# Performance work log

Hardware: AMD Instinct MI355X
Metric: run time of the kernel (lower is better)

Reference implementation:

```python
import jax, jax.numpy as jnp
import numpy as np

D_MODEL = 768
HEADS = 12
D_HEAD = D_MODEL // HEADS
D_DYNA = 768
EPS = 1e-5
B, SP, SI = 16, 256, 1024


def _layernorm(x, g, b):
    mu = jnp.mean(x, axis=-1, keepdims=True)
    var = jnp.var(x, axis=-1, keepdims=True)
    return (x - mu) * jax.lax.rsqrt(var + EPS) * g + b


def _mha(q, k, v, wq, bq, wk, bk, wv, bv, wo, bo):
    # weights stored [d_in, d_out]; torch Linear math y = x @ W^T + b is
    # equivalent with transposed storage.
    B_ = q.shape[0]
    qh = (q @ wq + bq).reshape(B_, -1, HEADS, D_HEAD)
    kh = (k @ wk + bk).reshape(B_, -1, HEADS, D_HEAD)
    vh = (v @ wv + bv).reshape(B_, -1, HEADS, D_HEAD)
    scores = jnp.einsum('bqhd,bkhd->bhqk', qh, kh) / np.sqrt(D_HEAD).astype(np.float32)
    attn = jax.nn.softmax(scores, axis=-1)  # dropout disabled (eval)
    out = jnp.einsum('bhqk,bkhd->bqhd', attn, vh).reshape(B_, -1, D_MODEL)
    return out @ wo + bo


def setup_inputs() -> dict:
    key = jax.random.key(0)
    ks = iter(jax.random.split(key, 40))
    s = 0.02
    d = {
        'image': jax.random.normal(next(ks), (B, SI, D_MODEL), jnp.float32),
        'prompt': jax.random.normal(next(ks), (B, SP, D_MODEL), jnp.float32),
        'posi': jax.random.normal(next(ks), (B, SI, D_MODEL), jnp.float32),
        'posp': jax.random.normal(next(ks), (B, SP, D_MODEL), jnp.float32),
    }
    for ln in ('ln_p1', 'ln_p2', 'ln_p3', 'ln_i1'):
        d[ln + '_g'] = jnp.ones((D_MODEL,), jnp.float32)
        d[ln + '_b'] = jnp.zeros((D_MODEL,), jnp.float32)
    for pre in ('pp', 'pi'):
        for nm in ('q', 'k', 'v', 'o'):
            d[f'{pre}_w{nm}'] = s * jax.random.normal(next(ks), (D_MODEL, D_MODEL), jnp.float32)
            d[f'{pre}_b{nm}'] = jnp.zeros((D_MODEL,), jnp.float32)
    d['ff_w1'] = s * jax.random.normal(next(ks), (D_MODEL, D_MODEL), jnp.float32)
    d['ff_b1'] = jnp.zeros((D_MODEL,), jnp.float32)
    d['ff_w2'] = s * jax.random.normal(next(ks), (D_MODEL, D_DYNA), jnp.float32)
    d['ff_b2'] = jnp.zeros((D_DYNA,), jnp.float32)
    return d


def reference(image, prompt, posi, posp,
              ln_p1_g, ln_p1_b, ln_p2_g, ln_p2_b, ln_p3_g, ln_p3_b, ln_i1_g, ln_i1_b,
              pp_wq, pp_bq, pp_wk, pp_bk, pp_wv, pp_bv, pp_wo, pp_bo,
              pi_wq, pi_bq, pi_wk, pi_bk, pi_wv, pi_bv, pi_wo, pi_bo,
              ff_w1, ff_b1, ff_w2, ff_b2):
    prompt0 = prompt + posp
    xp = _layernorm(prompt0, ln_p1_g, ln_p1_b)
    xp = _mha(xp, xp, xp, pp_wq, pp_bq, pp_wk, pp_bk, pp_wv, pp_bv, pp_wo, pp_bo)
    prompt = prompt + xp  # dropout_p1 is identity in eval
    xp = _layernorm(prompt + prompt0, ln_p2_g, ln_p2_b)
    xi = _layernorm(image + posi, ln_i1_g, ln_i1_b)
    xp = _mha(xp, xi, xi, pi_wq, pi_bq, pi_wk, pi_bk, pi_wv, pi_bv, pi_wo, pi_bo)
    prompt = prompt + xp  # dropout_p2 identity
    xp = _layernorm(prompt + prompt0, ln_p3_g, ln_p3_b)
    xp = jax.nn.relu(xp @ ff_w1 + ff_b1) @ ff_w2 + ff_b2
    return xp
```

## Files before the change

### kernel.cpp

```cpp
#include <hip/hip_runtime.h>
#include <hip/hip_bf16.h>
#include <stdint.h>
#include <math.h>

#define D_MODEL 768
#define HEADS 12
#define D_HEAD 64
#define BATCH 16
#define SP 256
#define SI 1024
#define NP (BATCH * SP)
#define NI (BATCH * SI)

#define GLOBAL_AS __attribute__((address_space(1)))
#define LDS_AS    __attribute__((address_space(3)))

typedef __attribute__((ext_vector_type(8))) short  frag_ab;
typedef __attribute__((ext_vector_type(4))) float  frag_cd;

static __device__ __forceinline__ ushort f2bf(float f) {
  __hip_bfloat16 h = __float2bfloat16(f);
  return *(ushort*)&h;
}
static __device__ __forceinline__ float bf2f(ushort u) {
  return __bfloat162float(*(__hip_bfloat16*)&u);
}
static __device__ __forceinline__ bool probe_bf(const uint32_t* p) {
  return p[0] == 0x3F803F80u;
}

struct Prep {
  const void* wsrc[10]; ushort* wdst[10];
  const void* vsrc[18]; float* vdst;
};

__global__ __launch_bounds__(256) void prep_kernel(Prep p, const uint32_t* probe) {
  const bool isbf = probe_bf(probe);
  const int z = blockIdx.z;
  if (z < 10) {
    __shared__ float tile[32][33];
    const int tx = threadIdx.x & 31, ty = threadIdx.x >> 5;
    const int x0 = blockIdx.x * 32, y0 = blockIdx.y * 32;
    const void* src = p.wsrc[z];
    ushort* dst = p.wdst[z];
#pragma unroll
    for (int i = 0; i < 4; i++) {
      const int y = y0 + ty + i * 8;
      float v;
      if (isbf) v = bf2f(((const ushort*)src)[(size_t)y * 768 + x0 + tx]);
      else      v = ((const float*)src)[(size_t)y * 768 + x0 + tx];
      tile[ty + i * 8][tx] = v;
    }
    __syncthreads();
#pragma unroll
    for (int i = 0; i < 4; i++) {
      const int row = x0 + ty + i * 8;
      const int col = y0 + tx;
      dst[(size_t)row * 768 + col] = f2bf(tile[tx][ty + i * 8]);
    }
  } else {
    const int idx = (blockIdx.y * 24 + blockIdx.x) * 256 + threadIdx.x;
    if (idx < 18 * 768) {
      const int e = idx / 768, i = idx - e * 768;
      float v;
      if (isbf) v = bf2f(((const ushort*)p.vsrc[e])[i]);
      else      v = ((const float*)p.vsrc[e])[i];
      p.vdst[idx] = v;
    }
  }
}

struct LNJob {
  const void* a; const void* b;
  const float* g; const float* be;
  float* sum_out; ushort* ln_out;
  int nrows; int abf;
};

__global__ __launch_bounds__(256) void add_ln_wave(LNJob J0, LNJob J1, const uint32_t* probe) {
  const int w = threadIdx.x >> 6, lane = threadIdx.x & 63;
  int row = blockIdx.x * 4 + w;
  LNJob j = (row < J0.nrows) ? J0 : J1;
  if (row >= J0.nrows) row -= J0.nrows;
  if (row >= j.nrows) return;
  const size_t base = (size_t)row * D_MODEL;
  const bool isbf = j.abf && probe_bf(probe);
  float x[12];
#pragma unroll
  for (int k = 0; k < 3; k++) {
    const int c = k * 256 + lane * 4;
    if (isbf) {
      const uint2 ua = *(const uint2*)((const ushort*)j.a + base + c);
      const uint2 ub = *(const uint2*)((const ushort*)j.b + base + c);
      const ushort* pa = (const ushort*)&ua;
      const ushort* pb = (const ushort*)&ub;
#pragma unroll
      for (int t = 0; t < 4; t++) x[k * 4 + t] = bf2f(pa[t]) + bf2f(pb[t]);
    } else {
      const float4 fa = *(const float4*)((const float*)j.a + base + c);
      const float4 fb = *(const float4*)((const float*)j.b + base + c);
      x[k * 4 + 0] = fa.x + fb.x; x[k * 4 + 1] = fa.y + fb.y;
      x[k * 4 + 2] = fa.z + fb.z; x[k * 4 + 3] = fa.w + fb.w;
    }
    if (j.sum_out) {
      float4 s4;
      s4.x = x[k * 4 + 0]; s4.y = x[k * 4 + 1];
      s4.z = x[k * 4 + 2]; s4.w = x[k * 4 + 3];
      *(float4*)&j.sum_out[base + c] = s4;
    }
  }
  float s = 0.f, q = 0.f;
#pragma unroll
  for (int t = 0; t < 12; t++) { s += x[t]; q += x[t] * x[t]; }
#pragma unroll
  for (int o = 32; o > 0; o >>= 1) { s += __shfl_xor(s, o); q += __shfl_xor(q, o); }
  const float mu  = s * (1.0f / D_MODEL);
  const float var = q * (1.0f / D_MODEL) - mu * mu;
  const float inv = rsqrtf(var + 1e-5f);
#pragma unroll
  for (int k = 0; k < 3; k++) {
    const int c = k * 256 + lane * 4;
    const float4 gv = *(const float4*)&j.g[c];
    const float4 bv = *(const float4*)&j.be[c];
    uint2 ou;
    ushort* oe = (ushort*)&ou;
    oe[0] = f2bf((x[k * 4 + 0] - mu) * inv * gv.x + bv.x);
    oe[1] = f2bf((x[k * 4 + 1] - mu) * inv * gv.y + bv.y);
    oe[2] = f2bf((x[k * 4 + 2] - mu) * inv * gv.z + bv.z);
    oe[3] = f2bf((x[k * 4 + 3] - mu) * inv * gv.w + bv.w);
    *(uint2*)(j.ln_out + base + c) = ou;
  }
}

#define BAR   __builtin_amdgcn_s_barrier()
#define LGKM0 do { asm volatile("s_waitcnt lgkmcnt(0)" ::: "memory"); \
                   __builtin_amdgcn_sched_barrier(0); } while (0)
#define VMC4  do { asm volatile("s_waitcnt vmcnt(4)" ::: "memory"); \
                   __builtin_amdgcn_sched_barrier(0); } while (0)
#define VMC8  do { asm volatile("s_waitcnt vmcnt(8)" ::: "memory"); \
                   __builtin_amdgcn_sched_barrier(0); } while (0)

#define RD_A(SL) do { \
  const ushort* _b = &lds[SL][0][0]; \
  _Pragma("unroll") for (int _m = 0; _m < 4; ++_m) \
  _Pragma("unroll") for (int _k = 0; _k < 2; ++_k) \
    aF[_m][_k] = *(const frag_ab*)(_b + ((wr << 6) + _m * 16 + ml) * 64 + \
                                   (((_k << 5) + (kq << 3)) ^ swz)); \
} while (0)

#define RD_B(DST, SL, no) do { \
  const ushort* _b = &lds[SL][1][0]; \
  _Pragma("unroll") for (int _n = 0; _n < 2; ++_n) \
  _Pragma("unroll") for (int _k = 0; _k < 2; ++_k) \
    DST[_n][_k] = *(const frag_ab*)(_b + ((wc << 6) + (no) + _n * 16 + ml) * 64 + \
                                    (((_k << 5) + (kq << 3)) ^ swz)); \
} while (0)

#define MM(NB, BF) do { \
  __builtin_amdgcn_s_setprio(1); \
  _Pragma("unroll") for (int _m = 0; _m < 4; ++_m) \
  _Pragma("unroll") for (int _n = 0; _n < 2; ++_n) \
  _Pragma("unroll") for (int _k = 0; _k < 2; ++_k) \
    acc[_m][(NB) + _n] = __builtin_amdgcn_mfma_f32_16x16x32_bf16( \
        aF[_m][_k], BF[_n][_k], acc[_m][(NB) + _n], 0, 0, 0); \
  __builtin_amdgcn_s_setprio(0); \
} while (0)

#define STAGE(SL, RG, PTR, RBASE, KT) do { \
  const ushort* _p = (PTR) + (size_t)((RBASE) + srow) * 768 + ((KT) << 6) + scol; \
  _Pragma("unroll") for (int _j = 0; _j < 4; ++_j) \
    __builtin_amdgcn_global_load_lds( \
        (const GLOBAL_AS void*)(_p + (size_t)(_j * 32) * 768), \
        (LDS_AS void*)((LDS_AS ushort*)&lds[SL][RG][0] + (((_j << 2) + w) << 9)), \
        16, 0, 0); \
} while (0)

#define ENGINE128() do { \
  STAGE(0, 0, jA, m0, 0); \
  STAGE(0, 1, jB, n0, 0); \
  STAGE(1, 0, jA, m0, 1); \
  VMC4; BAR; \
  for (int it = 0; it < 6; ++it) { \
    const int t1  = 2 * it + 1; \
    const int tn0 = (2 * it + 2 < 12) ? 2 * it + 2 : 11; \
    const int tn1 = (2 * it + 3 < 12) ? 2 * it + 3 : 11; \
    RD_A(0); RD_B(bF0, 0, 0); \
    STAGE(1, 1, jB, n0, t1); \
    LGKM0; \
    MM(0, bF0); \
    BAR; \
    RD_B(bF1, 0, 32); \
    STAGE(0, 0, jA, m0, tn0); \
    LGKM0; \
    MM(2, bF1); \
    VMC4; BAR; \
    RD_A(1); RD_B(bF0, 1, 0); \
    STAGE(0, 1, jB, n0, tn0); \
    LGKM0; \
    MM(0, bF0); \
    BAR; \
    RD_B(bF1, 1, 32); \
    STAGE(1, 0, jA, m0, tn1); \
    LGKM0; \
    MM(2, bF1); \
    VMC4; BAR; \
  } \
} while (0)

struct GJob {
  const ushort* A; const ushort* Bt; const float* bias;
  ushort* o0; ushort* o1; ushort* vT;
  int X; int vsub; int shift;
};

__global__ __launch_bounds__(256, 2) void gemm_mega128(GJob J0, GJob J1, int n0blocks) {
  __shared__ __align__(16) ushort lds[2][2][8192];
  int bid = blockIdx.x;
  GJob j = (bid < n0blocks) ? J0 : J1;
  if (bid >= n0blocks) bid -= n0blocks;
  const int tid  = threadIdx.x;
  const int lane = tid & 63, w = tid >> 6;
  const int wr = w >> 1, wc = w & 1;
  const int ml = lane & 15, kq = lane >> 4;
  const int rest = bid >> 3;
  const int x = rest % j.X, y = (bid & 7) + 8 * (rest / j.X);
  const int m0 = y << 7, n0 = x << 7;
  const int srow = (w << 3) + (lane >> 3);
  const int scol = (((lane & 7) ^ (lane >> 3)) << 3);
  const int swz  = (ml & 7) << 3;
  const ushort* jA = j.A;
  const ushort* jB = j.Bt;

  frag_cd acc[4][4] = {};
  frag_ab aF[4][2], bF0[2][2], bF1[2][2];

  ENGINE128();

  const int sub  = x / 6;
  const int mask = (1 << j.shift) - 1;
#pragma unroll
  for (int mt = 0; mt < 4; mt++) {
#pragma unroll
    for (int nt = 0; nt < 4; nt++) {
      const int row0 = m0 + wr * 64 + mt * 16 + kq * 4;
      const int col  = n0 + wc * 64 + nt * 16 + ml;
      const float bc = j.bias[col];
      if (sub == j.vsub) {
        const int hcol = col - sub * 768;
        const int hh = hcol >> 6, dd = hcol & 63;
        const int bb = row0 >> j.shift;
        const int jj = row0 & mask;
        uint2 pack;
        ushort* pe = (ushort*)&pack;
#pragma unroll
        for (int r = 0; r < 4; r++) pe[r] = f2bf(acc[mt][nt][r] + bc);
        *(uint2*)(j.vT + ((((size_t)(bb * HEADS + hh) << 6) + dd) << j.shift) + jj) = pack;
      } else {
        ushort* out = (sub == 0) ? j.o0 : j.o1;
        const int cl = col - sub * 768;
#pragma unroll
        for (int r = 0; r < 4; r++)
          out[(size_t)(row0 + r) * 768 + cl] = f2bf(acc[mt][nt][r] + bc);
      }
    }
  }
}

#undef RD_A
#undef RD_B
#undef MM
#undef STAGE
#undef ENGINE128

#define DRD_A(SL) do { \
  const ushort* _b = &lds[SL][0][0]; \
  _Pragma("unroll") for (int _m = 0; _m < 4; ++_m) \
  _Pragma("unroll") for (int _k = 0; _k < 2; ++_k) \
    aF[_m][_k] = *(const frag_ab*)(_b + ((wr << 6) + _m * 16 + ml) * 64 + \
                                   (((_k << 5) + (kq << 3)) ^ swz)); \
} while (0)

#define DRD_B(SL) do { \
  const ushort* _b = &lds[SL][1][0]; \
  _Pragma("unroll") for (int _n = 0; _n < 2; ++_n) \
  _Pragma("unroll") for (int _k = 0; _k < 2; ++_k) \
    bF[_n][_k] = *(const frag_ab*)(_b + ((wc << 5) + _n * 16 + ml) * 64 + \
                                   (((_k << 5) + (kq << 3)) ^ swz)); \
} while (0)

#define DMM() do { \
  __builtin_amdgcn_s_setprio(1); \
  _Pragma("unroll") for (int _m = 0; _m < 4; ++_m) \
  _Pragma("unroll") for (int _n = 0; _n < 2; ++_n) \
  _Pragma("unroll") for (int _k = 0; _k < 2; ++_k) \
    acc[_m][_n] = __builtin_amdgcn_mfma_f32_16x16x32_bf16( \
        aF[_m][_k], bF[_n][_k], acc[_m][_n], 0, 0, 0); \
  __builtin_amdgcn_s_setprio(0); \
} while (0)

#define DSTG(SL, RG, PTR, RBASE, KT) do { \
  const ushort* _p = (PTR) + (size_t)((RBASE) + srow) * 768 + ((KT) << 6) + scol; \
  __builtin_amdgcn_global_load_lds((const GLOBAL_AS void*)_p, \
      (LDS_AS void*)((LDS_AS ushort*)&lds[SL][RG][0] + (w << 9)), 16, 0, 0); \
  __builtin_amdgcn_global_load_lds((const GLOBAL_AS void*)(_p + (size_t)64 * 768), \
      (LDS_AS void*)((LDS_AS ushort*)&lds[SL][RG][0] + ((8 + w) << 9)), 16, 0, 0); \
} while (0)

__global__ __launch_bounds__(512, 1) void gemm_v3d(
    const ushort* __restrict__ A, const ushort* __restrict__ Bt,
    const float* __restrict__ bias,
    const void* __restrict__ resid, int rmode,
    void* __restrict__ C, int relu, int omode,
    const uint32_t* __restrict__ probe, int X) {
  __shared__ __align__(16) ushort lds[4][2][8192];
  const int bid  = blockIdx.x;
  const int tid  = threadIdx.x;
  const int lane = tid & 63, w = tid >> 6;
  const int wr = w >> 2, wc = w & 3;
  const int ml = lane & 15, kq = lane >> 4;
  const int rest = bid >> 3;
  const int x = rest % X, y = (bid & 7) + 8 * (rest / X);
  const int m0 = y << 7, n0 = x << 7;
  const int srow = (w << 3) + (lane >> 3);
  const int scol = (((lane & 7) ^ (lane >> 3)) << 3);
  const int swz  = (ml & 7) << 3;

  frag_cd acc[4][2] = {};
  frag_ab aF[4][2], bF[2][2];

  DSTG(0, 0, A, m0, 0); DSTG(0, 1, Bt, n0, 0);
  DSTG(1, 0, A, m0, 1); DSTG(1, 1, Bt, n0, 1);
  DSTG(2, 0, A, m0, 2); DSTG(2, 1, Bt, n0, 2);
  VMC8; BAR;

#pragma unroll 4
  for (int t = 0; t < 12; ++t) {
    const int sl  = t & 3;
    const int tn  = (t + 3 < 12) ? t + 3 : 11;
    const int sln = (t + 3) & 3;
    DSTG(sln, 0, A, m0, tn); DSTG(sln, 1, Bt, n0, tn);
    VMC8;
    DRD_A(sl); DRD_B(sl);
    LGKM0;
    DMM();
    BAR;
  }

  const bool obf = (omode == 1) || (omode == 2 && probe_bf(probe));
  const bool rbf = (rmode == 2) && probe_bf(probe);
#pragma unroll
  for (int mt = 0; mt < 4; mt++) {
#pragma unroll
    for (int nt = 0; nt < 2; nt++) {
      const int row0 = m0 + wr * 64 + mt * 16 + kq * 4;
      const int col  = n0 + wc * 32 + nt * 16 + ml;
      const float bc = bias[col];
#pragma unroll
      for (int r = 0; r < 4; r++) {
        const size_t off = (size_t)(row0 + r) * 768 + col;
        float v = acc[mt][nt][r] + bc;
        if (rmode != 0)
          v += rbf ? bf2f(((const ushort*)resid)[off]) : ((const float*)resid)[off];
        if (relu) v = fmaxf(v, 0.f);
        if (obf) ((ushort*)C)[off] = f2bf(v);
        else     ((float*)C)[off]  = v;
      }
    }
  }
}

#undef DRD_A
#undef DRD_B
#undef DMM
#undef DSTG

#define FS 68
__global__ __launch_bounds__(256) void fattn_mfma(
    const ushort* __restrict__ Q, const ushort* __restrict__ Kp,
    const ushort* __restrict__ vT, ushort* __restrict__ O, int Skv) {
  __shared__ __align__(16) ushort Qs[64 * FS];
  __shared__ __align__(16) ushort Ks[2][64 * FS];
  __shared__ __align__(16) ushort Vt[2][64 * FS];
  __shared__ __align__(16) ushort Ps[64 * FS];
  const int tid  = threadIdx.x;
  const int lane = tid & 63, w = tid >> 6;
  const int ml   = lane & 15, kq = lane >> 4;
  const int bid = blockIdx.x;
  const int g8  = bid & 7;
  const int qt  = (bid >> 3) & 3;
  const int g   = (bid >> 5) * 8 + g8;
  const int h   = g % HEADS;
  const int b   = g / HEADS;
  const int q0  = qt * 64;
  const ushort* Qb  = Q  + ((size_t)b * SP + q0) * D_MODEL + h * D_HEAD;
  const ushort* Kb  = Kp + (size_t)b * Skv * D_MODEL + h * D_HEAD;
  const ushort* vTb = vT + (size_t)g * 64 * Skv;

  const int r0 = tid >> 3, p0 = tid & 7;
  const int r1 = r0 + 32;

  for (int c = tid; c < 512; c += 256) {
    const int r = c >> 3, p = c & 7;
    *(uint4*)&Qs[r * FS + p * 8] = *(const uint4*)(Qb + (size_t)r * D_MODEL + p * 8);
  }

  uint4 kr0 = *(const uint4*)(Kb + (size_t)r0 * D_MODEL + p0 * 8);
  uint4 vr0 = *(const uint4*)(vTb + (size_t)r0 * Skv + p0 * 8);
  uint4 kr1 = *(const uint4*)(Kb + (size_t)r1 * D_MODEL + p0 * 8);
  uint4 vr1 = *(const uint4*)(vTb + (size_t)r1 * Skv + p0 * 8);
  *(uint4*)&Ks[0][r0 * FS + p0 * 8] = kr0;
  *(uint4*)&Vt[0][r0 * FS + p0 * 8] = vr0;
  *(uint4*)&Ks[0][r1 * FS + p0 * 8] = kr1;
  *(uint4*)&Vt[0][r1 * FS + p0 * 8] = vr1;
  __syncthreads();

  frag_ab qa[2];
#pragma unroll
  for (int kc = 0; kc < 2; kc++)
    qa[kc] = *(const frag_ab*)&Qs[(w * 16 + ml) * FS + kc * 32 + kq * 8];

  frag_cd oc[4] = {};
  float m_i[4], l_i[4];
#pragma unroll
  for (int r = 0; r < 4; r++) { m_i[r] = -1e30f; l_i[r] = 0.f; }
  const float SCL = 0.125f * 1.44269504f;
  const int NT = Skv >> 6;

  for (int t = 0; t < NT; ++t) {
    const int cb = t & 1;
    if (t + 1 < NT) {
      const int jn = (t + 1) << 6;
      kr0 = *(const uint4*)(Kb + (size_t)(jn + r0) * D_MODEL + p0 * 8);
      vr0 = *(const uint4*)(vTb + (size_t)r0 * Skv + jn + p0 * 8);
      kr1 = *(const uint4*)(Kb + (size_t)(jn + r1) * D_MODEL + p0 * 8);
      vr1 = *(const uint4*)(vTb + (size_t)r1 * Skv + jn + p0 * 8);
    }

    frag_cd sc[4] = {};
#pragma unroll
    for (int nt = 0; nt < 4; nt++)
#pragma unroll
      for (int kc = 0; kc < 2; kc++) {
        const frag_ab bfr = *(const frag_ab*)&Ks[cb][(nt * 16 + ml) * FS + kc * 32 + kq * 8];
        sc[nt] = __builtin_amdgcn_mfma_f32_16x16x32_bf16(qa[kc], bfr, sc[nt], 0, 0, 0);
      }
#pragma unroll
    for (int nt = 0; nt < 4; nt++)
#pragma unroll
      for (int r = 0; r < 4; r++) sc[nt][r] *= SCL;

    float al[4];
#pragma unroll
    for (int r = 0; r < 4; r++) {
      float mx = fmaxf(fmaxf(sc[0][r], sc[1][r]), fmaxf(sc[2][r], sc[3][r]));
#pragma unroll
      for (int m = 1; m < 16; m <<= 1) mx = fmaxf(mx, __shfl_xor(mx, m, 16));
      const float mnew = fmaxf(m_i[r], mx);
      al[r] = exp2f(m_i[r] - mnew);
      float p[4], s = 0.f;
#pragma unroll
      for (int nt = 0; nt < 4; nt++) { p[nt] = exp2f(sc[nt][r] - mnew); s += p[nt]; }
#pragma unroll
      for (int m = 1; m < 16; m <<= 1) s += __shfl_xor(s, m, 16);
      l_i[r] = l_i[r] * al[r] + s;
      m_i[r] = mnew;
      const int prow = (w * 16 + kq * 4 + r) * FS;
#pragma unroll
      for (int nt = 0; nt < 4; nt++) Ps[prow + nt * 16 + ml] = f2bf(p[nt]);
    }
#pragma unroll
    for (int dt = 0; dt < 4; dt++)
#pragma unroll
      for (int r = 0; r < 4; r++) oc[dt][r] *= al[r];

#pragma unroll
    for (int kc = 0; kc < 2; kc++) {
      const frag_ab pa = *(const frag_ab*)&Ps[(w * 16 + ml) * FS + kc * 32 + kq * 8];
#pragma unroll
      for (int dt = 0; dt < 4; dt++) {
        const frag_ab vb = *(const frag_ab*)&Vt[cb][(dt * 16 + ml) * FS + kc * 32 + kq * 8];
        oc[dt] = __builtin_amdgcn_mfma_f32_16x16x32_bf16(pa, vb, oc[dt], 0, 0, 0);
      }
    }

    if (t + 1 < NT) {
      *(uint4*)&Ks[cb ^ 1][r0 * FS + p0 * 8] = kr0;
      *(uint4*)&Vt[cb ^ 1][r0 * FS + p0 * 8] = vr0;
      *(uint4*)&Ks[cb ^ 1][r1 * FS + p0 * 8] = kr1;
      *(uint4*)&Vt[cb ^ 1][r1 * FS + p0 * 8] = vr1;
      __syncthreads();
    }
  }

  float inv[4];
#pragma unroll
  for (int r = 0; r < 4; r++) inv[r] = 1.0f / l_i[r];
#pragma unroll
  for (int dt = 0; dt < 4; dt++)
#pragma unroll
    for (int r = 0; r < 4; r++)
      O[((size_t)b * SP + q0 + w * 16 + kq * 4 + r) * D_MODEL + h * D_HEAD + dt * 16 + ml] =
          f2bf(oc[dt][r] * inv[r]);
}

extern "C" void kernel_launch(void* const* d_in, const int* in_sizes, int n_in,
                              void* d_out, int out_size, void* d_ws, size_t ws_size,
                              hipStream_t stream) {
  (void)in_sizes; (void)n_in; (void)out_size;
  char* base = (char*)d_ws;
  size_t off = 256;
  auto alloc = [&](size_t bytes) -> char* {
    char* p = base + off;
    off = (off + bytes + 255) & ~(size_t)255;
    return p;
  };
  const size_t WB = (size_t)768 * 768 * 2;
  ushort* Wt[10];
  for (int i = 0; i < 10; i++) Wt[i] = (ushort*)alloc(WB);
  float* vecs = (float*)alloc(18 * 768 * 4);
  float* biasF[10];
  for (int i = 0; i < 10; i++) biasF[i] = vecs + i * 768;
  float* lnF = vecs + 10 * 768;
  float* prompt0 = (float*)alloc((size_t)NP * 768 * 4);
  float* cur     = (float*)alloc((size_t)NP * 768 * 4);
  ushort* q_bf   = (ushort*)alloc((size_t)NP * 768 * 2);
  ushort* k_s    = (ushort*)alloc((size_t)NP * 768 * 2);
  ushort* k_c    = (ushort*)alloc((size_t)NI * 768 * 2);
  ushort* xln_bf = (ushort*)alloc((size_t)NP * 768 * 2);
  ushort* xi_bf  = (ushort*)alloc((size_t)NI * 768 * 2);
  ushort* obuf_bf = (ushort*)alloc((size_t)NP * 768 * 2);
  ushort* ffn1_bf = (ushort*)alloc((size_t)NP * 768 * 2);
  ushort* vT_s   = (ushort*)alloc((size_t)BATCH * HEADS * 64 * SP * 2);
  ushort* vT_c   = (ushort*)alloc((size_t)BATCH * HEADS * 64 * SI * 2);
  if (ws_size < off) return;

  const uint32_t* probe = (const uint32_t*)d_in[4];
  const int widx[10] = {12, 14, 16, 18, 20, 22, 24, 26, 28, 30};
  const int bidx[10] = {13, 15, 17, 19, 21, 23, 25, 27, 29, 31};

  Prep pr{};
  for (int i = 0; i < 10; i++) { pr.wsrc[i] = d_in[widx[i]]; pr.wdst[i] = Wt[i]; }
  for (int i = 0; i < 10; i++) pr.vsrc[i] = d_in[bidx[i]];
  for (int i = 0; i < 8;  i++) pr.vsrc[10 + i] = d_in[4 + i];
  pr.vdst = vecs;
  prep_kernel<<<dim3(24, 24, 11), 256, 0, stream>>>(pr, probe);

  float* G1 = lnF + 0 * 768, *B1 = lnF + 1 * 768;
  float* G2 = lnF + 2 * 768, *B2 = lnF + 3 * 768;
  float* G3 = lnF + 4 * 768, *B3 = lnF + 5 * 768;
  float* Gi = lnF + 6 * 768, *Bi = lnF + 7 * 768;

  LNJob L0{d_in[1], d_in[3], G1, B1, prompt0, xln_bf, NP, 1};
  LNJob Li{d_in[0], d_in[2], Gi, Bi, nullptr, xi_bf,  NI, 1};
  add_ln_wave<<<(NP + NI) / 4, 256, 0, stream>>>(L0, Li, probe);

  GJob js{xln_bf, Wt[0], biasF[0], q_bf, k_s, vT_s, 18, 2, 8};
  GJob jc{xi_bf,  Wt[5], biasF[5], k_c,  nullptr, vT_c, 12, 1, 10};
  gemm_mega128<<<576 + 1536, 256, 0, stream>>>(js, jc, 576);

  fattn_mfma<<<BATCH * HEADS * (SP / 64), 256, 0, stream>>>(q_bf, k_s, vT_s, obuf_bf, SP);

  gemm_v3d<<<192, 512, 0, stream>>>(obuf_bf, Wt[3], biasF[3],
      d_in[1], 2, cur, 0, 0, probe, 6);

  LNJob L2{cur, prompt0, G2, B2, nullptr, xln_bf, NP, 0};
  LNJob Lz{}; Lz.nrows = 0;
  add_ln_wave<<<NP / 4, 256, 0, stream>>>(L2, Lz, probe);

  gemm_v3d<<<192, 512, 0, stream>>>(xln_bf, Wt[4], biasF[4],
      nullptr, 0, q_bf, 0, 1, probe, 6);

  fattn_mfma<<<BATCH * HEADS * (SP / 64), 256, 0, stream>>>(q_bf, k_c, vT_c, obuf_bf, SI);

  gemm_v3d<<<192, 512, 0, stream>>>(obuf_bf, Wt[7], biasF[7],
      cur, 1, cur, 0, 0, probe, 6);

  LNJob L3{cur, prompt0, G3, B3, nullptr, xln_bf, NP, 0};
  add_ln_wave<<<NP / 4, 256, 0, stream>>>(L3, Lz, probe);

  gemm_v3d<<<192, 512, 0, stream>>>(xln_bf, Wt[8], biasF[8],
      nullptr, 0, ffn1_bf, 1, 1, probe, 6);

  gemm_v3d<<<192, 512, 0, stream>>>(ffn1_bf, Wt[9], biasF[9],
      nullptr, 0, d_out, 0, 2, probe, 6);
}
```

Baseline: 467.7 us.

## Rewrite fused QKV GEMM with 512 threads, K=32 steps and 4-stage ring

Replaces the 256-thread, double-buffered 128x128 GEMM with K-tile 64 by a 512-thread version. It uses eight waves (2x4, each 64x32), K-tile 32 and a four-slot LDS ring with loads issued three tiles ahead. The aim is more waves per CU and deeper prefetch to hide global-to-LDS latency. In exchange it pays one barrier per 32-wide K step, uses fewer MFMAs per wave per tile, and changes the LDS swizzle to a 4-way pattern that may cause bank conflicts.

Result: no change. 464.4 us (-0.7%).

```diff
diff --git a/kernel.cpp b/kernel.cpp
--- a/kernel.cpp
+++ b/kernel.cpp
@@ -140,110 +140,87 @@
 #define VMC8  do { asm volatile("s_waitcnt vmcnt(8)" ::: "memory"); \
                    __builtin_amdgcn_sched_barrier(0); } while (0)
 
-#define RD_A(SL) do { \
-  const ushort* _b = &lds[SL][0][0]; \
-  _Pragma("unroll") for (int _m = 0; _m < 4; ++_m) \
-  _Pragma("unroll") for (int _k = 0; _k < 2; ++_k) \
-    aF[_m][_k] = *(const frag_ab*)(_b + ((wr << 6) + _m * 16 + ml) * 64 + \
-                                   (((_k << 5) + (kq << 3)) ^ swz)); \
-} while (0)
-
-#define RD_B(DST, SL, no) do { \
-  const ushort* _b = &lds[SL][1][0]; \
-  _Pragma("unroll") for (int _n = 0; _n < 2; ++_n) \
-  _Pragma("unroll") for (int _k = 0; _k < 2; ++_k) \
-    DST[_n][_k] = *(const frag_ab*)(_b + ((wc << 6) + (no) + _n * 16 + ml) * 64 + \
-                                    (((_k << 5) + (kq << 3)) ^ swz)); \
-} while (0)
-
-#define MM(NB, BF) do { \
-  __builtin_amdgcn_s_setprio(1); \
-  _Pragma("unroll") for (int _m = 0; _m < 4; ++_m) \
-  _Pragma("unroll") for (int _n = 0; _n < 2; ++_n) \
-  _Pragma("unroll") for (int _k = 0; _k < 2; ++_k) \
-    acc[_m][(NB) + _n] = __builtin_amdgcn_mfma_f32_16x16x32_bf16( \
-        aF[_m][_k], BF[_n][_k], acc[_m][(NB) + _n], 0, 0, 0); \
-  __builtin_amdgcn_s_setprio(0); \
-} while (0)
-
-#define STAGE(SL, RG, PTR, RBASE, KT) do { \
-  const ushort* _p = (PTR) + (size_t)((RBASE) + srow) * 768 + ((KT) << 6) + scol; \
-  _Pragma("unroll") for (int _j = 0; _j < 4; ++_j) \
-    __builtin_amdgcn_global_load_lds( \
-        (const GLOBAL_AS void*)(_p + (size_t)(_j * 32) * 768), \
-        (LDS_AS void*)((LDS_AS ushort*)&lds[SL][RG][0] + (((_j << 2) + w) << 9)), \
-        16, 0, 0); \
-} while (0)
-
-#define ENGINE128() do { \
-  STAGE(0, 0, jA, m0, 0); \
-  STAGE(0, 1, jB, n0, 0); \
-  STAGE(1, 0, jA, m0, 1); \
-  VMC4; BAR; \
-  for (int it = 0; it < 6; ++it) { \
-    const int t1  = 2 * it + 1; \
-    const int tn0 = (2 * it + 2 < 12) ? 2 * it + 2 : 11; \
-    const int tn1 = (2 * it + 3 < 12) ? 2 * it + 3 : 11; \
-    RD_A(0); RD_B(bF0, 0, 0); \
-    STAGE(1, 1, jB, n0, t1); \
-    LGKM0; \
-    MM(0, bF0); \
-    BAR; \
-    RD_B(bF1, 0, 32); \
-    STAGE(0, 0, jA, m0, tn0); \
-    LGKM0; \
-    MM(2, bF1); \
-    VMC4; BAR; \
-    RD_A(1); RD_B(bF0, 1, 0); \
-    STAGE(0, 1, jB, n0, tn0); \
-    LGKM0; \
-    MM(0, bF0); \
-    BAR; \
-    RD_B(bF1, 1, 32); \
-    STAGE(1, 0, jA, m0, tn1); \
-    LGKM0; \
-    MM(2, bF1); \
-    VMC4; BAR; \
-  } \
-} while (0)
-
 struct GJob {
   const ushort* A; const ushort* Bt; const float* bias;
   ushort* o0; ushort* o1; ushort* vT;
   int X; int vsub; int shift;
 };
 
-__global__ __launch_bounds__(256, 2) void gemm_mega128(GJob J0, GJob J1, int n0blocks) {
-  __shared__ __align__(16) ushort lds[2][2][8192];
+#define MSTG(SL, RG, PTR, RBASE, KT) \
+  __builtin_amdgcn_global_load_lds( \
+      (const GLOBAL_AS void*)((PTR) + (size_t)((RBASE) + srow) * 768 + ((KT) << 5) + scol), \
+      (LDS_AS void*)((LDS_AS ushort*)&lds[SL][RG][0] + (w << 9)), 16, 0, 0)
+
+#define MRD_A(SL) do { \
+  const ushort* _b = &lds[SL][0][0]; \
+  _Pragma("unroll") for (int _m = 0; _m < 4; ++_m) \
+    aF[_m] = *(const frag_ab*)(_b + (((wr << 6) + _m * 16 + ml) << 5) + \
+                               ((kq << 3) ^ swz)); \
+} while (0)
+
+#define MRD_B(SL) do { \
+  const ushort* _b = &lds[SL][1][0]; \
+  _Pragma("unroll") for (int _n = 0; _n < 2; ++_n) \
+    bF[_n] = *(const frag_ab*)(_b + (((wc << 5) + _n * 16 + ml) << 5) + \
+                               ((kq << 3) ^ swz)); \
+} while (0)
+
+#define MMM() do { \
+  __builtin_amdgcn_s_setprio(1); \
+  _Pragma("unroll") for (int _m = 0; _m < 4; ++_m) \
+  _Pragma("unroll") for (int _n = 0; _n < 2; ++_n) \
+    acc[_m][_n] = __builtin_amdgcn_mfma_f32_16x16x32_bf16( \
+        aF[_m], bF[_n], acc[_m][_n], 0, 0, 0); \
+  __builtin_amdgcn_s_setprio(0); \
+} while (0)
+
+__global__ __launch_bounds__(512, 4) void gemm_mega32(GJob J0, GJob J1, int n0blocks) {
+  __shared__ __align__(16) ushort lds[4][2][4096];
   int bid = blockIdx.x;
   GJob j = (bid < n0blocks) ? J0 : J1;
   if (bid >= n0blocks) bid -= n0blocks;
   const int tid  = threadIdx.x;
   const int lane = tid & 63, w = tid >> 6;
-  const int wr = w >> 1, wc = w & 1;
+  const int wr = w >> 2, wc = w & 3;
   const int ml = lane & 15, kq = lane >> 4;
   const int rest = bid >> 3;
   const int x = rest % j.X, y = (bid & 7) + 8 * (rest / j.X);
   const int m0 = y << 7, n0 = x << 7;
-  const int srow = (w << 3) + (lane >> 3);
-  const int scol = (((lane & 7) ^ (lane >> 3)) << 3);
-  const int swz  = (ml & 7) << 3;
+  const int srow = tid >> 2;
+  const int scol = (((tid & 3) ^ ((tid >> 2) & 3)) << 3);
+  const int swz  = (ml & 3) << 3;
   const ushort* jA = j.A;
   const ushort* jB = j.Bt;
 
-  frag_cd acc[4][4] = {};
-  frag_ab aF[4][2], bF0[2][2], bF1[2][2];
-
-  ENGINE128();
+  frag_cd acc[4][2] = {};
+  frag_ab aF[4], bF[2];
+
+  MSTG(0, 0, jA, m0, 0); MSTG(0, 1, jB, n0, 0);
+  MSTG(1, 0, jA, m0, 1); MSTG(1, 1, jB, n0, 1);
+  MSTG(2, 0, jA, m0, 2); MSTG(2, 1, jB, n0, 2);
+  VMC4; BAR;
+
+#pragma unroll 4
+  for (int t = 0; t < 24; ++t) {
+    const int sl  = t & 3;
+    const int tn  = (t + 3 < 24) ? t + 3 : 23;
+    const int sln = (t + 3) & 3;
+    MSTG(sln, 0, jA, m0, tn); MSTG(sln, 1, jB, n0, tn);
+    VMC4;
+    MRD_A(sl); MRD_B(sl);
+    LGKM0;
+    MMM();
+    BAR;
+  }
 
   const int sub  = x / 6;
   const int mask = (1 << j.shift) - 1;
 #pragma unroll
   for (int mt = 0; mt < 4; mt++) {
 #pragma unroll
-    for (int nt = 0; nt < 4; nt++) {
-      const int row0 = m0 + wr * 64 + mt * 16 + kq * 4;
-      const int col  = n0 + wc * 64 + nt * 16 + ml;
+    for (int nt = 0; nt < 2; nt++) {
+      const int row0 = m0 + (wr << 6) + mt * 16 + kq * 4;
+      const int col  = n0 + (wc << 5) + nt * 16 + ml;
       const float bc = j.bias[col];
       if (sub == j.vsub) {
         const int hcol = col - sub * 768;
@@ -266,11 +243,10 @@
   }
 }
 
-#undef RD_A
-#undef RD_B
-#undef MM
-#undef STAGE
-#undef ENGINE128
+#undef MSTG
+#undef MRD_A
+#undef MRD_B
+#undef MMM
 
 #define DRD_A(SL) do { \
   const ushort* _b = &lds[SL][0][0]; \
@@ -556,7 +532,7 @@
 
   GJob js{xln_bf, Wt[0], biasF[0], q_bf, k_s, vT_s, 18, 2, 8};
   GJob jc{xi_bf,  Wt[5], biasF[5], k_c,  nullptr, vT_c, 12, 1, 10};
-  gemm_mega128<<<576 + 1536, 256, 0, stream>>>(js, jc, 576);
+  gemm_mega32<<<576 + 1536, 512, 0, stream>>>(js, jc, 576);
 
   fattn_mfma<<<BATCH * HEADS * (SP / 64), 256, 0, stream>>>(q_bf, k_s, vT_s, obuf_bf, SP);
 
```
